# Performance work log

Measured on AMD Instinct MI355X. Metric: run time of the kernel, lower is better.

## Reference

```python
import jax, jax.numpy as jnp
import numpy as np


def setup_inputs() -> dict:
    key = jax.random.key(0)
    k1, k2 = jax.random.split(key)
    B, C, H, W, T = 8, 256, 64, 64, 512
    F_s = jax.random.normal(k1, (B, C, H, W), dtype=jnp.float32)
    F_t = jax.random.normal(k2, (B, T, C), dtype=jnp.float32)
    return {"F_s": F_s, "F_t": F_t}


def reference(F_s, F_t):
    B, C, H, W = F_s.shape
    T = F_t.shape[1]
    # [B, HW, C] spatial tokens
    F_s_t = jnp.transpose(F_s, (0, 2, 3, 1)).reshape(B, H * W, C)
    # scores [B, HW, T], scaled by sqrt(T) (softmax over last axis)
    A = jnp.einsum('bnc,btc->bnt', F_s_t, F_t) / jnp.sqrt(jnp.float32(T))
    A = jax.nn.softmax(A, axis=-1)
    # A^T @ F_s_t -> updated text tokens [B, T, C]
    F_t_updated = jnp.einsum('bnt,bnc->btc', A, F_s_t)
    # A @ F_t -> spatial update [B, HW, C]
    F_s_t_update = jnp.einsum('bnt,btc->bnc', A, F_t)
    F_s_t_update = jnp.transpose(F_s_t_update.reshape(B, H, W, C), (0, 3, 1, 2))
    F_s_updated = F_s + F_s_t_update
    return (F_s_updated, F_t_updated)
```

## Files before the change

kernel.cpp:

```cpp
#include <hip/hip_runtime.h>
#include <hip/hip_bf16.h>
#include <stdint.h>


typedef __attribute__((ext_vector_type(8))) short short8v;
typedef __attribute__((ext_vector_type(4))) float float4v;

#define MFMA16(a, b, c) __builtin_amdgcn_mfma_f32_16x16x32_bf16(a, b, c, 0, 0, 0)
#define SCALE 0.04419417382415922f

static __device__ __forceinline__ unsigned short f2bf(float f) {
  union { float f; uint32_t u; } v; v.f = f;
  uint32_t r = v.u + 0x7fffu + ((v.u >> 16) & 1u);
  return (unsigned short)(r >> 16);
}
static __device__ __forceinline__ float bf2f(unsigned short u) {
  union { uint32_t u; float f; } v; v.u = (uint32_t)u << 16;
  return v.f;
}

static __device__ __forceinline__ void gload16(const void* g, void* l) {
  __builtin_amdgcn_global_load_lds(
      (const __attribute__((address_space(1))) void*)g,
      (__attribute__((address_space(3))) void*)l, 16, 0, 0);
}

__global__ __launch_bounds__(256) void k_cast_transpose(
    const float* __restrict__ src, unsigned short* __restrict__ dstC,
    unsigned short* __restrict__ dstT, int R, int Cd) {
  __shared__ unsigned short tile[32][33];
  const size_t zoff = (size_t)blockIdx.z * R * Cd;
  const float* s = src + zoff;
  unsigned short* dc = dstC + zoff;
  unsigned short* dt = dstT + zoff;
  const int c0 = blockIdx.x * 32, r0 = blockIdx.y * 32;
  const int tid = threadIdx.x;
  const int r = tid >> 3, c4 = (tid & 7) * 4;

  float4 v = *(const float4*)&s[(size_t)(r0 + r) * Cd + c0 + c4];
  ushort4 bq;
  bq.x = f2bf(v.x); bq.y = f2bf(v.y); bq.z = f2bf(v.z); bq.w = f2bf(v.w);
  *(ushort4*)&dc[(size_t)(r0 + r) * Cd + c0 + c4] = bq;
  tile[r][c4 + 0] = bq.x; tile[r][c4 + 1] = bq.y;
  tile[r][c4 + 2] = bq.z; tile[r][c4 + 3] = bq.w;
  __syncthreads();
  ushort4 o;
  o.x = tile[c4 + 0][r]; o.y = tile[c4 + 1][r];
  o.z = tile[c4 + 2][r]; o.w = tile[c4 + 3][r];
  *(ushort4*)&dt[(size_t)(c0 + r) * R + r0 + c4] = o;
}

__global__ __launch_bounds__(256, 2) void k_attn(
    const unsigned short* __restrict__ Qg, const unsigned short* __restrict__ Kg,
    const unsigned short* __restrict__ VTg, const unsigned short* __restrict__ QTg,
    float* __restrict__ out0, unsigned short* __restrict__ PTg) {
  __shared__ char smem[81920];

  const int tid = threadIdx.x;
  const int wave = tid >> 6, lane = tid & 63;
  const int l16 = lane & 15, lhi = lane >> 4;
  const int b = blockIdx.x & 7, nb = blockIdx.x >> 3;
  const int n0w = nb * 64 + wave * 16;
  const int cx = (l16 & 7) << 4;

  const unsigned short* Qb = Qg + (size_t)b * 4096 * 256;
  const char* Kb = (const char*)(Kg + (size_t)b * 512 * 256);
  const char* VTb = (const char*)(VTg + (size_t)b * 256 * 512);

#define STAGE_K16(c_) do {                                                  \
    const char* src_ = Kb + (c_) * 16384;                                   \
    char* dst_ = smem + ((c_) & 3) * 16384;                                 \
    _Pragma("unroll")                                                       \
    for (int i = 0; i < 4; i++) {                                           \
      const int off = (tid + i * 256) * 16;                                 \
      gload16(src_ + (off ^ (((off >> 9) & 7) << 4)), dst_ + off);          \
    } } while (0)

#define STAGE_VT16(v_) do {                                                 \
    const int ch_ = (v_) & 1, tau_ = (v_) >> 1;                             \
    char* dst_ = smem + ((v_) & 3) * 16384;                                 \
    _Pragma("unroll")                                                       \
    for (int i = 0; i < 4; i++) {                                           \
      const int off = (tid + i * 256) * 16;                                 \
      const int r_ = off >> 7, ic_ = off & 127;                             \
      gload16(VTb + (size_t)(ch_ * 128 + r_) * 1024 + tau_ * 128            \
                  + (ic_ ^ ((r_ & 7) << 4)),                                \
              dst_ + off);                                                  \
    } } while (0)

  short8v aQ[8];
#pragma unroll
  for (int kc = 0; kc < 8; kc++)
    aQ[kc] = *(const short8v*)(Qb + (size_t)(n0w + l16) * 256 + kc * 32 + lhi * 8);

  float4v acc[32];
#pragma unroll
  for (int tt = 0; tt < 32; tt++) acc[tt] = (float4v)0.f;

  STAGE_K16(0); STAGE_K16(1); STAGE_K16(2);
#pragma unroll
  for (int c = 0; c < 16; c++) {
    asm volatile("s_waitcnt vmcnt(8)" ::: "memory");
    __builtin_amdgcn_s_barrier();
    if (c < 13) STAGE_K16(c + 3);
    else        STAGE_VT16(c - 13);
    const char* bufp = smem + (c & 3) * 16384;
#pragma unroll
    for (int ti = 0; ti < 2; ti++) {
      const char* rb = bufp + (ti * 16 + l16) * 512;
#pragma unroll
      for (int kc = 0; kc < 8; kc++) {
        short8v bf = *(const short8v*)(rb + ((kc * 64 + lhi * 16) ^ cx));
        acc[c * 2 + ti] = MFMA16(aQ[kc], bf, acc[c * 2 + ti]);
      }
    }
    asm volatile("s_waitcnt lgkmcnt(0)" ::: "memory");
  }

  float mx[4], sm[4];
#pragma unroll
  for (int r = 0; r < 4; r++) {
    float m = acc[0][r];
#pragma unroll
    for (int tt = 1; tt < 32; tt++) m = fmaxf(m, acc[tt][r]);
    m = fmaxf(m, __shfl_xor(m, 1));
    m = fmaxf(m, __shfl_xor(m, 2));
    m = fmaxf(m, __shfl_xor(m, 4));
    m = fmaxf(m, __shfl_xor(m, 8));
    mx[r] = m;
  }
#pragma unroll
  for (int r = 0; r < 4; r++) {
    float s = 0.f;
#pragma unroll
    for (int tt = 0; tt < 32; tt++) {
      float p = __expf((acc[tt][r] - mx[r]) * SCALE);
      acc[tt][r] = p;
      s += p;
    }
    s += __shfl_xor(s, 1); s += __shfl_xor(s, 2);
    s += __shfl_xor(s, 4); s += __shfl_xor(s, 8);
    sm[r] = 1.0f / s;
  }

  uint32_t pk[64];
#pragma unroll
  for (int tt = 0; tt < 32; tt++)
#pragma unroll
    for (int h = 0; h < 2; h++)
      pk[tt * 2 + h] = (uint32_t)f2bf(acc[tt][2 * h] * sm[2 * h]) |
                       ((uint32_t)f2bf(acc[tt][2 * h + 1] * sm[2 * h + 1]) << 16);

  float4v oacc[16];
#pragma unroll
  for (int ct = 0; ct < 16; ct++) oacc[ct] = (float4v)0.f;

  unsigned short* PTb = PTg + (size_t)b * 512 * 4096;
  short8v pb0 = short8v{}, pb1 = short8v{};

#pragma unroll
  for (int v = 0; v < 16; v++) {
    if (v <= 13)      asm volatile("s_waitcnt vmcnt(8)" ::: "memory");
    else if (v == 14) asm volatile("s_waitcnt vmcnt(4)" ::: "memory");
    else              asm volatile("s_waitcnt vmcnt(0)" ::: "memory");
    __builtin_amdgcn_s_barrier();
    if (v < 13) STAGE_VT16(v + 3);
    const int tau = v >> 1, ch = v & 1;
    char* Psb = smem + 65536 + (tau & 1) * 8192 + wave * 2048;
    if (ch == 0) {
#pragma unroll
      for (int s = 0; s < 4; s++)
#pragma unroll
        for (int r = 0; r < 4; r++) {
          const int q = lhi * 4 + r, t2 = s * 16 + l16;
          const uint32_t w = pk[(tau * 4 + s) * 2 + (r >> 1)];
          *(unsigned short*)(Psb + ((q * 128 + t2 * 2) ^ ((q & 7) << 4))) =
              (unsigned short)(w >> ((r & 1) * 16));
        }
      pb0 = *(const short8v*)(Psb + ((l16 * 128 + lhi * 16) ^ cx));
      pb1 = *(const short8v*)(Psb + ((l16 * 128 + 64 + lhi * 16) ^ cx));
    }
    const char* bufp = smem + (v & 3) * 16384;
#pragma unroll
    for (int ctl = 0; ctl < 8; ctl++) {
      const char* rb = bufp + (ctl * 16 + l16) * 128;
      short8v a0 = *(const short8v*)(rb + ((lhi * 16) ^ cx));
      oacc[ch * 8 + ctl] = MFMA16(a0, pb0, oacc[ch * 8 + ctl]);
      short8v a1 = *(const short8v*)(rb + ((64 + lhi * 16) ^ cx));
      oacc[ch * 8 + ctl] = MFMA16(a1, pb1, oacc[ch * 8 + ctl]);
    }
    if (ch == 1) {
      const int t2 = lane;
      unsigned short tmp[16];
#pragma unroll
      for (int q = 0; q < 16; q++)
        tmp[q] = *(const unsigned short*)(Psb + ((q * 128 + t2 * 2) ^ ((q & 7) << 4)));
      *(int4*)(PTb + (size_t)(tau * 64 + t2) * 4096 + n0w) = *(int4*)&tmp[0];
      *(int4*)(PTb + (size_t)(tau * 64 + t2) * 4096 + n0w + 8) = *(int4*)&tmp[8];
    }
    asm volatile("s_waitcnt lgkmcnt(0)" ::: "memory");
  }

  const unsigned short* QTb = QTg + (size_t)b * 256 * 4096;
  float* o0 = out0 + (size_t)b * 256 * 4096;
#pragma unroll
  for (int ct = 0; ct < 16; ct++)
#pragma unroll
    for (int r = 0; r < 4; r++) {
      const int cgl = ct * 16 + lhi * 4 + r;
      const size_t off = (size_t)cgl * 4096 + n0w + l16;
      o0[off] = oacc[ct][r] + bf2f(QTb[off]);
    }
#undef STAGE_K16
#undef STAGE_VT16
}

__global__ __launch_bounds__(256, 2) void k_ptq(
    const unsigned short* __restrict__ PTg, const unsigned short* __restrict__ QTg,
    float* __restrict__ part) {
  __shared__ char smem[65536];

  const int tid = threadIdx.x;
  const int wave = tid >> 6, lane = tid & 63;
  const int l16 = lane & 15, lhi = lane >> 4;
  const int bid = blockIdx.x;
  const int t0 = (bid >> 6) * 64;
  const int grp = bid & 63;
  const int b = grp & 7, ksl = grp >> 3;
  const int cx = (l16 & 7) << 4;

  const unsigned short* PTrow =
      PTg + ((size_t)(b * 512 + t0 + wave * 16 + l16)) * 4096 + ksl * 512 + lhi * 8;
  const char* QTb = (const char*)(QTg + (size_t)b * 256 * 4096 + ksl * 512);

#define STAGE_Q(c_, buf_) do {                                              \
    _Pragma("unroll")                                                       \
    for (int i = 0; i < 8; i++) {                                           \
      const int off = (tid + i * 256) * 16;                                 \
      const int r_ = off >> 7, ic_ = off & 127;                             \
      gload16(QTb + (size_t)r_ * 8192 + (c_) * 128 + (ic_ ^ ((r_ & 7) << 4)), \
              smem + (buf_) * 32768 + off);                                 \
    } } while (0)

  float4v acc[16];
#pragma unroll
  for (int ct = 0; ct < 16; ct++) acc[ct] = (float4v)0.f;

  STAGE_Q(0, 0);
  __syncthreads();
#pragma unroll
  for (int c = 0; c < 8; c++) {
    const int buf = c & 1;
    short8v pa0 = *(const short8v*)(PTrow + c * 64);
    short8v pa1 = *(const short8v*)(PTrow + c * 64 + 32);
    if (c < 7) STAGE_Q(c + 1, buf ^ 1);
#pragma unroll
    for (int ct = 0; ct < 16; ct++) {
      const int row = ct * 16 + l16;
      const char* rb = smem + buf * 32768 + row * 128;
      short8v b0 = *(const short8v*)(rb + ((lhi * 16) ^ cx));
      acc[ct] = MFMA16(pa0, b0, acc[ct]);
      short8v b1 = *(const short8v*)(rb + ((64 + lhi * 16) ^ cx));
      acc[ct] = MFMA16(pa1, b1, acc[ct]);
    }
    __syncthreads();
  }

  float* pout = part + (((size_t)ksl * 8 + b) * 512 + t0 + wave * 16) * 256;
#pragma unroll
  for (int ct = 0; ct < 16; ct++)
#pragma unroll
    for (int r = 0; r < 4; r++)
      pout[(lhi * 4 + r) * 256 + ct * 16 + l16] = acc[ct][r];
#undef STAGE_Q
}

__global__ __launch_bounds__(256) void k_red(
    const float* __restrict__ part, float* __restrict__ out1) {
  const int g = blockIdx.x * 256 + threadIdx.x;
  float4 s = *(const float4*)(part + (size_t)g * 4);
#pragma unroll
  for (int ksl = 1; ksl < 8; ksl++) {
    float4 v = *(const float4*)(part + (size_t)ksl * 1048576 + (size_t)g * 4);
    s.x += v.x; s.y += v.y; s.z += v.z; s.w += v.w;
  }
  *(float4*)(out1 + (size_t)g * 4) = s;
}

extern "C" void kernel_launch(void* const* d_in, const int* in_sizes, int n_in,
                              void* d_out, int out_size, void* d_ws, size_t ws_size,
                              hipStream_t stream) {
  const float* Fs = (const float*)d_in[0];
  const float* Ft = (const float*)d_in[1];
  float* out0 = (float*)d_out;
  float* out1 = out0 + (size_t)8 * 256 * 4096;

  unsigned short* ws = (unsigned short*)d_ws;
  unsigned short* Q  = ws;
  unsigned short* QT = Q + 8388608;
  unsigned short* K  = QT + 8388608;
  unsigned short* VT = K + 1048576;
  unsigned short* PT = VT + 1048576;
  float* part = (float*)(PT + 16777216);

  k_cast_transpose<<<dim3(128, 8, 8), 256, 0, stream>>>(Fs, QT, Q, 256, 4096);
  k_cast_transpose<<<dim3(8, 16, 8), 256, 0, stream>>>(Ft, K, VT, 512, 256);
  k_attn<<<dim3(512), 256, 0, stream>>>(Q, K, VT, QT, out0, PT);
  k_ptq<<<dim3(512), 256, 0, stream>>>(PT, QT, part);
  k_red<<<dim3(1024), 256, 0, stream>>>(part, out1);
}
```

Measured before the change: 81.92 us.

## Retile attention waves as 2x2 query-by-key grid with cross-wave softmax reduction

```diff
diff --git a/kernel.cpp b/kernel.cpp
--- a/kernel.cpp
+++ b/kernel.cpp
@@ -59,8 +59,9 @@
   const int tid = threadIdx.x;
   const int wave = tid >> 6, lane = tid & 63;
   const int l16 = lane & 15, lhi = lane >> 4;
+  const int wq = wave >> 1, wt = wave & 1;
   const int b = blockIdx.x & 7, nb = blockIdx.x >> 3;
-  const int n0w = nb * 64 + wave * 16;
+  const int n0 = nb * 64;
   const int cx = (l16 & 7) << 4;
 
   const unsigned short* Qb = Qg + (size_t)b * 4096 * 256;
@@ -88,14 +89,34 @@
               dst_ + off);                                                  \
     } } while (0)
 
-  short8v aQ[8];
-#pragma unroll
-  for (int kc = 0; kc < 8; kc++)
-    aQ[kc] = *(const short8v*)(Qb + (size_t)(n0w + l16) * 256 + kc * 32 + lhi * 8);
-
-  float4v acc[32];
-#pragma unroll
-  for (int tt = 0; tt < 32; tt++) acc[tt] = (float4v)0.f;
+#define PS_WRITE(tau_) do {                                                 \
+    char* PsN = smem + 65536 + ((tau_) & 1) * 8192 + wq * 4096;             \
+    _Pragma("unroll")                                                       \
+    for (int qt = 0; qt < 2; qt++)                                          \
+      _Pragma("unroll")                                                     \
+      for (int cc = 0; cc < 2; cc++)                                        \
+        _Pragma("unroll")                                                   \
+        for (int r = 0; r < 4; r++) {                                       \
+          const int q = qt * 16 + lhi * 4 + r;                              \
+          const int t2 = cc * 32 + wt * 16 + l16;                           \
+          const uint32_t w = pk[(qt * 16 + (tau_) * 2 + cc) * 2 + (r >> 1)];\
+          *(unsigned short*)(PsN + ((q * 128 + t2 * 2) ^ ((q & 7) << 4))) = \
+              (unsigned short)(w >> ((r & 1) * 16));                        \
+        } } while (0)
+
+  short8v aQ[2][8];
+#pragma unroll
+  for (int qt = 0; qt < 2; qt++)
+#pragma unroll
+    for (int kc = 0; kc < 8; kc++)
+      aQ[qt][kc] = *(const short8v*)(Qb +
+          (size_t)(n0 + wq * 32 + qt * 16 + l16) * 256 + kc * 32 + lhi * 8);
+
+  float4v acc[2][16];
+#pragma unroll
+  for (int qt = 0; qt < 2; qt++)
+#pragma unroll
+    for (int c = 0; c < 16; c++) acc[qt][c] = (float4v)0.f;
 
   STAGE_K16(0); STAGE_K16(1); STAGE_K16(2);
 #pragma unroll
@@ -104,59 +125,101 @@
     __builtin_amdgcn_s_barrier();
     if (c < 13) STAGE_K16(c + 3);
     else        STAGE_VT16(c - 13);
-    const char* bufp = smem + (c & 3) * 16384;
-#pragma unroll
-    for (int ti = 0; ti < 2; ti++) {
-      const char* rb = bufp + (ti * 16 + l16) * 512;
-#pragma unroll
-      for (int kc = 0; kc < 8; kc++) {
-        short8v bf = *(const short8v*)(rb + ((kc * 64 + lhi * 16) ^ cx));
-        acc[c * 2 + ti] = MFMA16(aQ[kc], bf, acc[c * 2 + ti]);
-      }
+    const char* rb = smem + (c & 3) * 16384 + (wt * 16 + l16) * 512;
+#pragma unroll
+    for (int kc = 0; kc < 8; kc++) {
+      short8v bf = *(const short8v*)(rb + ((kc * 64 + lhi * 16) ^ cx));
+      acc[0][c] = MFMA16(aQ[0][kc], bf, acc[0][c]);
+      acc[1][c] = MFMA16(aQ[1][kc], bf, acc[1][c]);
     }
     asm volatile("s_waitcnt lgkmcnt(0)" ::: "memory");
   }
 
-  float mx[4], sm[4];
-#pragma unroll
-  for (int r = 0; r < 4; r++) {
-    float m = acc[0][r];
-#pragma unroll
-    for (int tt = 1; tt < 32; tt++) m = fmaxf(m, acc[tt][r]);
-    m = fmaxf(m, __shfl_xor(m, 1));
-    m = fmaxf(m, __shfl_xor(m, 2));
-    m = fmaxf(m, __shfl_xor(m, 4));
-    m = fmaxf(m, __shfl_xor(m, 8));
-    mx[r] = m;
-  }
-#pragma unroll
-  for (int r = 0; r < 4; r++) {
-    float s = 0.f;
-#pragma unroll
-    for (int tt = 0; tt < 32; tt++) {
-      float p = __expf((acc[tt][r] - mx[r]) * SCALE);
-      acc[tt][r] = p;
-      s += p;
-    }
-    s += __shfl_xor(s, 1); s += __shfl_xor(s, 2);
-    s += __shfl_xor(s, 4); s += __shfl_xor(s, 8);
-    sm[r] = 1.0f / s;
-  }
+  float* red = (float*)(smem + 65536 + 8192);
+  float mx[2][4];
+#pragma unroll
+  for (int qt = 0; qt < 2; qt++)
+#pragma unroll
+    for (int r = 0; r < 4; r++) {
+      float m = acc[qt][0][r];
+#pragma unroll
+      for (int c = 1; c < 16; c++) m = fmaxf(m, acc[qt][c][r]);
+      m = fmaxf(m, __shfl_xor(m, 1));
+      m = fmaxf(m, __shfl_xor(m, 2));
+      m = fmaxf(m, __shfl_xor(m, 4));
+      m = fmaxf(m, __shfl_xor(m, 8));
+      mx[qt][r] = m;
+    }
+  if (l16 == 0) {
+#pragma unroll
+    for (int qt = 0; qt < 2; qt++)
+#pragma unroll
+      for (int r = 0; r < 4; r++)
+        red[(wq * 2 + wt) * 32 + qt * 16 + lhi * 4 + r] = mx[qt][r];
+  }
+  __builtin_amdgcn_s_barrier();
+  asm volatile("s_waitcnt lgkmcnt(0)" ::: "memory");
+#pragma unroll
+  for (int qt = 0; qt < 2; qt++)
+#pragma unroll
+    for (int r = 0; r < 4; r++) {
+      const int q = qt * 16 + lhi * 4 + r;
+      mx[qt][r] = fmaxf(red[(wq * 2 + 0) * 32 + q], red[(wq * 2 + 1) * 32 + q]);
+    }
+  float sm[2][4];
+#pragma unroll
+  for (int qt = 0; qt < 2; qt++)
+#pragma unroll
+    for (int r = 0; r < 4; r++) {
+      float s = 0.f;
+#pragma unroll
+      for (int c = 0; c < 16; c++) {
+        float p = __expf((acc[qt][c][r] - mx[qt][r]) * SCALE);
+        acc[qt][c][r] = p;
+        s += p;
+      }
+      s += __shfl_xor(s, 1); s += __shfl_xor(s, 2);
+      s += __shfl_xor(s, 4); s += __shfl_xor(s, 8);
+      sm[qt][r] = s;
+    }
+  if (l16 == 0) {
+#pragma unroll
+    for (int qt = 0; qt < 2; qt++)
+#pragma unroll
+      for (int r = 0; r < 4; r++)
+        red[128 + (wq * 2 + wt) * 32 + qt * 16 + lhi * 4 + r] = sm[qt][r];
+  }
+  __builtin_amdgcn_s_barrier();
+  asm volatile("s_waitcnt lgkmcnt(0)" ::: "memory");
+#pragma unroll
+  for (int qt = 0; qt < 2; qt++)
+#pragma unroll
+    for (int r = 0; r < 4; r++) {
+      const int q = qt * 16 + lhi * 4 + r;
+      sm[qt][r] = 1.0f / (red[128 + (wq * 2 + 0) * 32 + q] +
+                          red[128 + (wq * 2 + 1) * 32 + q]);
+    }
 
   uint32_t pk[64];
 #pragma unroll
-  for (int tt = 0; tt < 32; tt++)
-#pragma unroll
-    for (int h = 0; h < 2; h++)
-      pk[tt * 2 + h] = (uint32_t)f2bf(acc[tt][2 * h] * sm[2 * h]) |
-                       ((uint32_t)f2bf(acc[tt][2 * h + 1] * sm[2 * h + 1]) << 16);
-
-  float4v oacc[16];
-#pragma unroll
-  for (int ct = 0; ct < 16; ct++) oacc[ct] = (float4v)0.f;
+  for (int qt = 0; qt < 2; qt++)
+#pragma unroll
+    for (int c = 0; c < 16; c++)
+#pragma unroll
+      for (int h = 0; h < 2; h++)
+        pk[(qt * 16 + c) * 2 + h] =
+            (uint32_t)f2bf(acc[qt][c][2 * h] * sm[qt][2 * h]) |
+            ((uint32_t)f2bf(acc[qt][c][2 * h + 1] * sm[qt][2 * h + 1]) << 16);
+
+  PS_WRITE(0);
+
+  float4v oacc[8][2];
+#pragma unroll
+  for (int ct = 0; ct < 8; ct++)
+#pragma unroll
+    for (int qt = 0; qt < 2; qt++) oacc[ct][qt] = (float4v)0.f;
 
   unsigned short* PTb = PTg + (size_t)b * 512 * 4096;
-  short8v pb0 = short8v{}, pb1 = short8v{};
 
 #pragma unroll
   for (int v = 0; v < 16; v++) {
@@ -166,37 +229,42 @@
     __builtin_amdgcn_s_barrier();
     if (v < 13) STAGE_VT16(v + 3);
     const int tau = v >> 1, ch = v & 1;
-    char* Psb = smem + 65536 + (tau & 1) * 8192 + wave * 2048;
-    if (ch == 0) {
-#pragma unroll
-      for (int s = 0; s < 4; s++)
-#pragma unroll
-        for (int r = 0; r < 4; r++) {
-          const int q = lhi * 4 + r, t2 = s * 16 + l16;
-          const uint32_t w = pk[(tau * 4 + s) * 2 + (r >> 1)];
-          *(unsigned short*)(Psb + ((q * 128 + t2 * 2) ^ ((q & 7) << 4))) =
-              (unsigned short)(w >> ((r & 1) * 16));
+    char* PsT = smem + 65536 + (tau & 1) * 8192 + wq * 4096;
+    if (ch == wt) {
+      short8v pb00 = *(const short8v*)(PsT + (((0 * 16 + l16) * 128 + 0 * 64 + lhi * 16) ^ cx));
+      short8v pb01 = *(const short8v*)(PsT + (((0 * 16 + l16) * 128 + 1 * 64 + lhi * 16) ^ cx));
+      short8v pb10 = *(const short8v*)(PsT + (((1 * 16 + l16) * 128 + 0 * 64 + lhi * 16) ^ cx));
+      short8v pb11 = *(const short8v*)(PsT + (((1 * 16 + l16) * 128 + 1 * 64 + lhi * 16) ^ cx));
+      const char* bufp = smem + (v & 3) * 16384;
+#pragma unroll
+      for (int ct = 0; ct < 8; ct++) {
+        const char* rb = bufp + (ct * 16 + l16) * 128;
+        short8v a0 = *(const short8v*)(rb + ((lhi * 16) ^ cx));
+        oacc[ct][0] = MFMA16(a0, pb00, oacc[ct][0]);
+        oacc[ct][1] = MFMA16(a0, pb10, oacc[ct][1]);
+        short8v a1 = *(const short8v*)(rb + ((64 + lhi * 16) ^ cx));
+        oacc[ct][0] = MFMA16(a1, pb01, oacc[ct][0]);
+        oacc[ct][1] = MFMA16(a1, pb11, oacc[ct][1]);
+      }
+    }
+    if (ch == 1) {
+      if (tau < 7) {
+        const int taun = tau + 1;
+        PS_WRITE(taun);
+      }
+      {
+        const int t2 = wt * 32 + (lane & 31);
+        const int cg = (lane >> 5) * 16;
+        unsigned short tmp[16];
+#pragma unroll
+        for (int j = 0; j < 16; j++) {
+          const int q = cg + j;
+          tmp[j] = *(const unsigned short*)(PsT + ((q * 128 + t2 * 2) ^ ((q & 7) << 4)));
         }
-      pb0 = *(const short8v*)(Psb + ((l16 * 128 + lhi * 16) ^ cx));
-      pb1 = *(const short8v*)(Psb + ((l16 * 128 + 64 + lhi * 16) ^ cx));
-    }
-    const char* bufp = smem + (v & 3) * 16384;
-#pragma unroll
-    for (int ctl = 0; ctl < 8; ctl++) {
-      const char* rb = bufp + (ctl * 16 + l16) * 128;
-      short8v a0 = *(const short8v*)(rb + ((lhi * 16) ^ cx));
-      oacc[ch * 8 + ctl] = MFMA16(a0, pb0, oacc[ch * 8 + ctl]);
-      short8v a1 = *(const short8v*)(rb + ((64 + lhi * 16) ^ cx));
-      oacc[ch * 8 + ctl] = MFMA16(a1, pb1, oacc[ch * 8 + ctl]);
-    }
-    if (ch == 1) {
-      const int t2 = lane;
-      unsigned short tmp[16];
-#pragma unroll
-      for (int q = 0; q < 16; q++)
-        tmp[q] = *(const unsigned short*)(Psb + ((q * 128 + t2 * 2) ^ ((q & 7) << 4)));
-      *(int4*)(PTb + (size_t)(tau * 64 + t2) * 4096 + n0w) = *(int4*)&tmp[0];
-      *(int4*)(PTb + (size_t)(tau * 64 + t2) * 4096 + n0w + 8) = *(int4*)&tmp[8];
+        unsigned short* dst = PTb + (size_t)(tau * 64 + t2) * 4096 + n0 + wq * 32 + cg;
+        *(int4*)dst = *(int4*)&tmp[0];
+        *(int4*)(dst + 8) = *(int4*)&tmp[8];
+      }
     }
     asm volatile("s_waitcnt lgkmcnt(0)" ::: "memory");
   }
@@ -204,15 +272,19 @@
   const unsigned short* QTb = QTg + (size_t)b * 256 * 4096;
   float* o0 = out0 + (size_t)b * 256 * 4096;
 #pragma unroll
-  for (int ct = 0; ct < 16; ct++)
-#pragma unroll
-    for (int r = 0; r < 4; r++) {
-      const int cgl = ct * 16 + lhi * 4 + r;
-      const size_t off = (size_t)cgl * 4096 + n0w + l16;
-      o0[off] = oacc[ct][r] + bf2f(QTb[off]);
-    }
+  for (int ct = 0; ct < 8; ct++)
+#pragma unroll
+    for (int qt = 0; qt < 2; qt++)
+#pragma unroll
+      for (int r = 0; r < 4; r++) {
+        const int cgl = wt * 128 + ct * 16 + lhi * 4 + r;
+        const int n = n0 + wq * 32 + qt * 16 + l16;
+        const size_t off = (size_t)cgl * 4096 + n;
+        o0[off] = oacc[ct][qt][r] + bf2f(QTb[off]);
+      }
 #undef STAGE_K16
 #undef STAGE_VT16
+#undef PS_WRITE
 }
 
 __global__ __launch_bounds__(256, 2) void k_ptq(
```

New measurement: 79.32 us. 3.2% less time.
